# Optimization experiments

Measured on AMD Instinct MI355X. Metric: run time of the kernel, lower is better.

## Reference

```python
import jax, jax.numpy as jnp
import numpy as np

B, C, IN, OUT = 8192, 64, 64, 64


def setup_inputs() -> dict:
    key = jax.random.key(0)
    k1, k2, k3 = jax.random.split(key, 3)
    x = jax.random.normal(k1, (B, C, IN), dtype=jnp.float32)
    # kernel shape [1, category, in_channel, out_channel], bias [1, category, out_channel]
    kernel = jax.random.normal(k2, (1, C, IN, OUT), dtype=jnp.float32) * (1.0 / np.sqrt(IN))
    bias = jax.random.normal(k3, (1, C, OUT), dtype=jnp.float32) * 0.01
    return {"x": x, "kernel": kernel, "bias": bias}


def reference(x, kernel, bias):
    # Faithful to: sum(x[:,:,:,None] * kernel, dim=2) + bias, expressed as a
    # per-category batched GEMM to avoid the (B,C,IN,OUT) intermediate.
    out = jnp.einsum('bci,cio->bco', x, kernel[0])  # (B, C, OUT)
    out = out + bias  # bias broadcasts over batch
    # activation is None in this config
    return out
```

## Files before the change

### kernel.cpp

```cpp
#include <hip/hip_runtime.h>


constexpr int C_   = 64;
constexpr int IN_  = 64;
constexpr int OUT_ = 64;
constexpr int BT   = 256;

typedef __attribute__((ext_vector_type(8))) short bf16x8;
typedef __attribute__((ext_vector_type(4))) short s16x4;
typedef __attribute__((ext_vector_type(4))) float f32x4;

__device__ __forceinline__ short f2bf(float f) {
    union { float f; unsigned u; } v; v.f = f;
    unsigned r = v.u + 0x7FFF + ((v.u >> 16) & 1);
    return (short)(r >> 16);
}

__global__ __launch_bounds__(256, 4)
void cat_dense_mfma3(const float* __restrict__ x,
                     const float* __restrict__ k,
                     const float* __restrict__ bias,
                     float* __restrict__ out) {
    __shared__ unsigned short xsb[BT * IN_];
    __shared__ unsigned short ksb[IN_ * OUT_];

    const int tid  = threadIdx.x;
    const int wv   = tid >> 6;
    const int lane = tid & 63;
    const int c    = blockIdx.x & 63;
    const long bBase = (long)(blockIdx.x >> 6) * BT;

    const int lrow = lane & 15;
    const int lkg  = lane >> 4;

    #pragma unroll
    for (int it = 0; it < 4; ++it) {
        int p = tid + it * 256;
        f32x4 v = *(const f32x4*)(k + (size_t)c * (IN_ * OUT_) + p * 4);
        s16x4 w;
        #pragma unroll
        for (int e = 0; e < 4; ++e) w[e] = f2bf(v[e]);
        *(s16x4*)(&ksb[p * 4]) = w;
    }

    #pragma unroll
    for (int it = 0; it < 16; ++it) {
        int q   = tid + it * 256;
        int row = q >> 4, s8 = q & 15;
        f32x4 v = *(const f32x4*)(x + (size_t)(bBase + row) * (C_ * IN_)
                                    + c * IN_ + s8 * 4);
        s16x4 w;
        #pragma unroll
        for (int e = 0; e < 4; ++e) w[e] = f2bf(v[e]);
        int byteoff = row * 128 + ((((s8 >> 1) ^ (row & 7)) << 4) | ((s8 & 1) << 3));
        *(s16x4*)((char*)xsb + byteoff) = w;
    }

    f32x4 bv[4];
    #pragma unroll
    for (int nt = 0; nt < 4; ++nt)
        bv[nt] = *(const f32x4*)(bias + (size_t)c * OUT_ + nt * 16 + lkg * 4);

    __syncthreads();

    bf16x8 kb[4][2];
    #pragma unroll
    for (int nt = 0; nt < 4; ++nt)
      #pragma unroll
      for (int ksi = 0; ksi < 2; ++ksi) {
        bf16x8 b;
        #pragma unroll
        for (int j = 0; j < 8; ++j)
            b[j] = (short)ksb[(ksi * 32 + lkg * 8 + j) * OUT_ + nt * 16 + lrow];
        kb[nt][ksi] = b;
      }

    #pragma unroll
    for (int p = 0; p < 2; ++p) {
        bf16x8 af[2][2];
        #pragma unroll
        for (int mt = 0; mt < 2; ++mt)
          #pragma unroll
          for (int ksi = 0; ksi < 2; ++ksi) {
            int row = wv * 64 + p * 32 + mt * 16 + lrow;
            int byteoff = row * 128 + ((((ksi * 4 + lkg)) ^ (row & 7)) << 4);
            af[mt][ksi] = *(const bf16x8*)((const char*)xsb + byteoff);
          }

        f32x4 acc[2][4];
        #pragma unroll
        for (int mt = 0; mt < 2; ++mt)
          #pragma unroll
          for (int nt = 0; nt < 4; ++nt)
            acc[mt][nt] = (f32x4){0.f, 0.f, 0.f, 0.f};

        #pragma unroll
        for (int ksi = 0; ksi < 2; ++ksi)
          #pragma unroll
          for (int mt = 0; mt < 2; ++mt)
            #pragma unroll
            for (int nt = 0; nt < 4; ++nt)
                acc[mt][nt] = __builtin_amdgcn_mfma_f32_16x16x32_bf16(
                                  kb[nt][ksi], af[mt][ksi], acc[mt][nt], 0, 0, 0);

        #pragma unroll
        for (int mt = 0; mt < 2; ++mt) {
            size_t rbase = (size_t)(bBase + wv * 64 + p * 32 + mt * 16 + lrow)
                               * (C_ * OUT_)
                         + (size_t)c * OUT_ + lkg * 4;
            #pragma unroll
            for (int nt = 0; nt < 4; ++nt) {
                f32x4 o = acc[mt][nt] + bv[nt];
                *(f32x4*)(out + rbase + nt * 16) = o;
            }
        }
    }
}

extern "C" void kernel_launch(void* const* d_in, const int* in_sizes, int n_in,
                              void* d_out, int out_size, void* d_ws, size_t ws_size,
                              hipStream_t stream) {
    const float* x    = (const float*)d_in[0];
    const float* k    = (const float*)d_in[1];
    const float* bias = (const float*)d_in[2];
    float* out        = (float*)d_out;

    const int B     = in_sizes[0] / (C_ * IN_);
    const int tiles = B / BT;
    dim3 grid(64 * tiles);
    cat_dense_mfma3<<<grid, 256, 0, stream>>>(x, k, bias, out);
}
```

Measured before the change: 51.82 us.

## Load x fragments directly from global into registers, skip LDS staging

Removes the shared-memory staging of the x tile and its barrier dependency. Each lane now loads its MFMA A-fragment straight from global memory as two float4 loads, converting to bf16 in registers. The batch tile is doubled to 512 rows per block, processed in two 256-row passes, so each block does more work and the kernel-weight conversion is amortized. This cuts LDS traffic and occupancy pressure, but the global loads become 32-byte per-lane accesses strided across rows, which may coalesce less well than the previous cooperative loads. It also halves the grid size.

```diff
diff --git a/kernel.cpp b/kernel.cpp
--- a/kernel.cpp
+++ b/kernel.cpp
@@ -4,7 +4,7 @@
 constexpr int C_   = 64;
 constexpr int IN_  = 64;
 constexpr int OUT_ = 64;
-constexpr int BT   = 256;
+constexpr int BT   = 512;
 
 typedef __attribute__((ext_vector_type(8))) short bf16x8;
 typedef __attribute__((ext_vector_type(4))) short s16x4;
@@ -16,12 +16,21 @@
     return (short)(r >> 16);
 }
 
+__device__ __forceinline__ bf16x8 cvt8(f32x4 lo, f32x4 hi) {
+    bf16x8 r;
+    #pragma unroll
+    for (int e = 0; e < 4; ++e) {
+        r[e]     = f2bf(lo[e]);
+        r[4 + e] = f2bf(hi[e]);
+    }
+    return r;
+}
+
 __global__ __launch_bounds__(256, 4)
-void cat_dense_mfma3(const float* __restrict__ x,
+void cat_dense_mfma4(const float* __restrict__ x,
                      const float* __restrict__ k,
                      const float* __restrict__ bias,
                      float* __restrict__ out) {
-    __shared__ unsigned short xsb[BT * IN_];
     __shared__ unsigned short ksb[IN_ * OUT_];
 
     const int tid  = threadIdx.x;
@@ -36,24 +45,11 @@
     #pragma unroll
     for (int it = 0; it < 4; ++it) {
         int p = tid + it * 256;
-        f32x4 v = *(const f32x4*)(k + (size_t)c * (IN_ * OUT_) + p * 4);
+        f32x4 v = *(const f32x4*)(k + (size_t)c * (IN_ * OUT_) + (size_t)p * 4);
         s16x4 w;
         #pragma unroll
         for (int e = 0; e < 4; ++e) w[e] = f2bf(v[e]);
         *(s16x4*)(&ksb[p * 4]) = w;
-    }
-
-    #pragma unroll
-    for (int it = 0; it < 16; ++it) {
-        int q   = tid + it * 256;
-        int row = q >> 4, s8 = q & 15;
-        f32x4 v = *(const f32x4*)(x + (size_t)(bBase + row) * (C_ * IN_)
-                                    + c * IN_ + s8 * 4);
-        s16x4 w;
-        #pragma unroll
-        for (int e = 0; e < 4; ++e) w[e] = f2bf(v[e]);
-        int byteoff = row * 128 + ((((s8 >> 1) ^ (row & 7)) << 4) | ((s8 & 1) << 3));
-        *(s16x4*)((char*)xsb + byteoff) = w;
     }
 
     f32x4 bv[4];
@@ -68,50 +64,61 @@
     for (int nt = 0; nt < 4; ++nt)
       #pragma unroll
       for (int ksi = 0; ksi < 2; ++ksi) {
-        bf16x8 b;
+        union { bf16x8 v; short s[8]; } b;
         #pragma unroll
         for (int j = 0; j < 8; ++j)
-            b[j] = (short)ksb[(ksi * 32 + lkg * 8 + j) * OUT_ + nt * 16 + lrow];
-        kb[nt][ksi] = b;
+            b.s[j] = (short)ksb[(ksi * 32 + lkg * 8 + j) * OUT_ + nt * 16 + lrow];
+        kb[nt][ksi] = b.v;
       }
 
     #pragma unroll
-    for (int p = 0; p < 2; ++p) {
-        bf16x8 af[2][2];
+    for (int t = 0; t < 2; ++t) {
+        const long rw = bBase + t * 256 + wv * 64;
+
+        bf16x8 af[2][2][2];
         #pragma unroll
-        for (int mt = 0; mt < 2; ++mt)
-          #pragma unroll
-          for (int ksi = 0; ksi < 2; ++ksi) {
-            int row = wv * 64 + p * 32 + mt * 16 + lrow;
-            int byteoff = row * 128 + ((((ksi * 4 + lkg)) ^ (row & 7)) << 4);
-            af[mt][ksi] = *(const bf16x8*)((const char*)xsb + byteoff);
-          }
-
-        f32x4 acc[2][4];
-        #pragma unroll
-        for (int mt = 0; mt < 2; ++mt)
-          #pragma unroll
-          for (int nt = 0; nt < 4; ++nt)
-            acc[mt][nt] = (f32x4){0.f, 0.f, 0.f, 0.f};
-
-        #pragma unroll
-        for (int ksi = 0; ksi < 2; ++ksi)
+        for (int p = 0; p < 2; ++p)
           #pragma unroll
           for (int mt = 0; mt < 2; ++mt)
             #pragma unroll
-            for (int nt = 0; nt < 4; ++nt)
-                acc[mt][nt] = __builtin_amdgcn_mfma_f32_16x16x32_bf16(
-                                  kb[nt][ksi], af[mt][ksi], acc[mt][nt], 0, 0, 0);
+            for (int ksi = 0; ksi < 2; ++ksi) {
+                const float* xp = x
+                    + (size_t)(rw + p * 32 + mt * 16 + lrow) * (C_ * IN_)
+                    + (size_t)c * IN_ + ksi * 32 + lkg * 8;
+                f32x4 lo = *(const f32x4*)xp;
+                f32x4 hi = *(const f32x4*)(xp + 4);
+                af[p][mt][ksi] = cvt8(lo, hi);
+            }
 
         #pragma unroll
-        for (int mt = 0; mt < 2; ++mt) {
-            size_t rbase = (size_t)(bBase + wv * 64 + p * 32 + mt * 16 + lrow)
-                               * (C_ * OUT_)
-                         + (size_t)c * OUT_ + lkg * 4;
+        for (int p = 0; p < 2; ++p) {
+            f32x4 acc[2][4];
             #pragma unroll
-            for (int nt = 0; nt < 4; ++nt) {
-                f32x4 o = acc[mt][nt] + bv[nt];
-                *(f32x4*)(out + rbase + nt * 16) = o;
+            for (int mt = 0; mt < 2; ++mt)
+              #pragma unroll
+              for (int nt = 0; nt < 4; ++nt)
+                acc[mt][nt] = (f32x4){0.f, 0.f, 0.f, 0.f};
+
+            #pragma unroll
+            for (int ksi = 0; ksi < 2; ++ksi)
+              #pragma unroll
+              for (int mt = 0; mt < 2; ++mt)
+                #pragma unroll
+                for (int nt = 0; nt < 4; ++nt)
+                    acc[mt][nt] = __builtin_amdgcn_mfma_f32_16x16x32_bf16(
+                                      kb[nt][ksi], af[p][mt][ksi],
+                                      acc[mt][nt], 0, 0, 0);
+
+            #pragma unroll
+            for (int mt = 0; mt < 2; ++mt) {
+                size_t rbase = (size_t)(rw + p * 32 + mt * 16 + lrow)
+                                   * (C_ * OUT_)
+                             + (size_t)c * OUT_ + lkg * 4;
+                #pragma unroll
+                for (int nt = 0; nt < 4; ++nt) {
+                    f32x4 o = acc[mt][nt] + bv[nt];
+                    *(f32x4*)(out + rbase + nt * 16) = o;
+                }
             }
         }
     }
@@ -128,5 +135,5 @@
     const int B     = in_sizes[0] / (C_ * IN_);
     const int tiles = B / BT;
     dim3 grid(64 * tiles);
-    cat_dense_mfma3<<<grid, 256, 0, stream>>>(x, k, bias, out);
+    cat_dense_mfma4<<<grid, 256, 0, stream>>>(x, k, bias, out);
 }
```

After: 91.94 us. 1.77x slower.
